# Kernel optimization log

Hardware: AMD Instinct MI355X
Metric: run time of the kernel (lower is better)

The kernel has to match this reference:

```python
import math
import jax, jax.numpy as jnp
import numpy as np

T, B, F = 2048, 8, 768
N_HEAD = 12            # only used for the scale, per original code
N_CHUNK = 3            # chunk(3, -1) -> 3 effective heads
SCALE = math.sqrt(F // N_HEAD)  # sqrt(64) = 8.0


def setup_inputs() -> dict:
    key = jax.random.key(0)
    ks = jax.random.split(key, 9)
    s = 1.0 / math.sqrt(F)
    return {
        "x": jax.random.normal(ks[0], (T, B, F), jnp.float32),
        "Wq": jax.random.normal(ks[1], (F, F), jnp.float32) * s,
        "bq": jax.random.normal(ks[2], (F,), jnp.float32) * s,
        "Wk": jax.random.normal(ks[3], (F, F), jnp.float32) * s,
        "bk": jax.random.normal(ks[4], (F,), jnp.float32) * s,
        "Wv": jax.random.normal(ks[5], (F, F), jnp.float32) * s,
        "bv": jax.random.normal(ks[6], (F,), jnp.float32) * s,
        "Wo": jax.random.normal(ks[7], (F, F), jnp.float32) * s,
        "bo": jax.random.normal(ks[8], (F,), jnp.float32) * s,
    }


def reference(x, Wq, bq, Wk, bk, Wv, bv, Wo, bo):
    # x: (T, B, F). Linear is y = x @ W.T + b (torch convention).
    t, b, f = x.shape
    dh = f // N_CHUNK
    scale = jnp.asarray(SCALE, x.dtype)
    # project then split into 3 chunks along feature dim -> (T, B, 3, dh)
    q = (x @ Wq.T + bq).reshape(t, b, N_CHUNK, dh)
    k = (x @ Wk.T + bk).reshape(t, b, N_CHUNK, dh)
    v = (x @ Wv.T + bv).reshape(t, b, N_CHUNK, dh)
    # scores: (B, H, T, T)
    scores = jnp.einsum('tbhd,sbhd->bhts', q, k) / scale
    attn = jax.nn.softmax(scores, axis=-1)
    # output: (T, B, H, dh) -> (T, B, F)
    o = jnp.einsum('bhts,sbhd->tbhd', attn, v).reshape(t, b, f)
    return o @ Wo.T + bo
```

## Files before the change

kernel.cpp:

```cpp
#include <hip/hip_runtime.h>
#include <cstdint>
#include <cstddef>

#define T_SEQ 2048
#define B_SZ  8
#define F_DIM 768
#define H_CNT 3
#define DH    256

typedef float floatx4 __attribute__((ext_vector_type(4)));
typedef short bf16x8  __attribute__((ext_vector_type(8)));

static __device__ __forceinline__ unsigned short f2bf(float f) {
    union { float f; unsigned int i; } x; x.f = f;
    return (unsigned short)((x.i + 0x8000u) >> 16);
}
static __device__ __forceinline__ unsigned int pkbf(float a, float b) {
    union { float f; unsigned int i; } xa, xb; xa.f = a; xb.f = b;
    return __builtin_amdgcn_perm(xb.i + 0x8000u, xa.i + 0x8000u, 0x07060302u);
}
static __device__ __forceinline__ bf16x8 cvt8(const float* __restrict__ p) {
    const floatx4 a = *(const floatx4*)p;
    const floatx4 b = *(const floatx4*)(p + 4);
    union { unsigned int u[4]; bf16x8 v; } r;
    r.u[0] = pkbf(a[0], a[1]); r.u[1] = pkbf(a[2], a[3]);
    r.u[2] = pkbf(b[0], b[1]); r.u[3] = pkbf(b[2], b[3]);
    return r.v;
}

#define ASYNC16(g, l) __builtin_amdgcn_global_load_lds( \
    (__attribute__((address_space(1))) void*)(void*)(g), \
    (__attribute__((address_space(3))) void*)(l), 16, 0, 0)

template<int AMODE, int CMODE>
__global__ __launch_bounds__(256, 2) void gemm_nt(
    const void* __restrict__ Av,
    const float* __restrict__ W,
    const float* __restrict__ bias,
    void* __restrict__ Cv,
    int M, int N, int K, float scale)
{
    __shared__ __align__(16) unsigned short As[128 * 32];
    __shared__ __align__(16) unsigned short Bs[128 * 32];

    const int tid  = threadIdx.x;
    const int wave = tid >> 6;
    const int lane = tid & 63;
    const int m0 = blockIdx.y * 128;
    const int n0 = blockIdx.x * 128;
    const int wm = (wave >> 1) * 64;
    const int wn = (wave & 1) * 64;
    const int q4 = lane >> 4;
    const int rr = lane & 15;

    const int lrow = lane >> 2;
    const int lk8  = (lane & 3) * 8;
    const int ar0 = wave * 16 + lrow;
    const int ar1 = (wave + 4) * 16 + lrow;

    floatx4 acc[4][4];
#pragma unroll
    for (int i = 0; i < 4; ++i)
#pragma unroll
        for (int j = 0; j < 4; ++j) acc[i][j] = (floatx4)0.0f;

    for (int k0 = 0; k0 < K; k0 += 32) {
        bf16x8 a0, a1;
        if (AMODE == 0) {
            const float* A = (const float*)Av;
            a0 = cvt8(A + (size_t)(m0 + ar0) * K + k0 + lk8);
            a1 = cvt8(A + (size_t)(m0 + ar1) * K + k0 + lk8);
        }
        bf16x8 b0 = cvt8(W + (size_t)(n0 + ar0) * K + k0 + lk8);
        bf16x8 b1 = cvt8(W + (size_t)(n0 + ar1) * K + k0 + lk8);
        __syncthreads();
        if (AMODE == 0) {
            *(bf16x8*)&As[ar0 * 32 + lk8] = a0;
            *(bf16x8*)&As[ar1 * 32 + lk8] = a1;
        } else {
            const unsigned short* A = (const unsigned short*)Av;
            ASYNC16(A + (size_t)(m0 + ar0) * K + k0 + lk8, (unsigned short*)As + wave * 512);
            ASYNC16(A + (size_t)(m0 + ar1) * K + k0 + lk8, (unsigned short*)As + (wave + 4) * 512);
        }
        *(bf16x8*)&Bs[ar0 * 32 + lk8] = b0;
        *(bf16x8*)&Bs[ar1 * 32 + lk8] = b1;
        __syncthreads();

        bf16x8 af[4], bfv[4];
#pragma unroll
        for (int mt = 0; mt < 4; ++mt)
            af[mt] = *(const bf16x8*)&As[(wm + mt * 16 + rr) * 32 + q4 * 8];
#pragma unroll
        for (int nt = 0; nt < 4; ++nt)
            bfv[nt] = *(const bf16x8*)&Bs[(wn + nt * 16 + rr) * 32 + q4 * 8];
#pragma unroll
        for (int mt = 0; mt < 4; ++mt)
#pragma unroll
            for (int nt = 0; nt < 4; ++nt)
                acc[mt][nt] = __builtin_amdgcn_mfma_f32_16x16x32_bf16(af[mt], bfv[nt], acc[mt][nt], 0, 0, 0);
    }

#pragma unroll
    for (int nt = 0; nt < 4; ++nt) {
        const int col = n0 + wn + nt * 16 + rr;
        const float bv = bias[col];
#pragma unroll
        for (int mt = 0; mt < 4; ++mt) {
#pragma unroll
            for (int r = 0; r < 4; ++r) {
                const int row = m0 + wm + mt * 16 + q4 * 4 + r;
                const float v = (acc[mt][nt][r] + bv) * scale;
                if (CMODE == 2) {
                    ((float*)Cv)[(size_t)row * N + col] = v;
                } else {
                    const int t = row >> 3, bb = row & 7;
                    const int h = col >> 8, d = col & 255;
                    const size_t hb = (size_t)(bb * H_CNT + h) * (T_SEQ * DH);
                    size_t idx;
                    if (CMODE == 3) {
                        const int sblk = t >> 4, rrq = t & 15;
                        const int kc = d >> 5, q4v = (d >> 3) & 3, e = d & 7;
                        idx = hb + (size_t)(((sblk * 8 + kc) * 64 + q4v * 16 + rrq) * 8 + e);
                    } else {
                        const int skc = t >> 5, q4v = (t >> 3) & 3, e = t & 7;
                        const int dblk = d >> 4, rrq = d & 15;
                        idx = hb + (size_t)(((skc * 16 + dblk) * 64 + q4v * 16 + rrq) * 8 + e);
                    }
                    ((unsigned short*)Cv)[idx] = f2bf(v);
                }
            }
        }
    }
}

__global__ __launch_bounds__(128, 2) void attn_kernel(
    const unsigned short* __restrict__ Qf,
    const unsigned short* __restrict__ Kf,
    const unsigned short* __restrict__ Vf,
    unsigned short* __restrict__ Ob)
{
    __shared__ __align__(16) unsigned short Ks[8192];
    __shared__ __align__(16) unsigned short Vs[8192];
    __shared__ __align__(16) unsigned short Ps[2][32 * 40];

    const int tid  = threadIdx.x;
    const int wave = tid >> 6;
    const int lane = tid & 63;
    const int q4 = lane >> 4;
    const int rr = lane & 15;
    const int bh = blockIdx.y;
    const int b  = bh / H_CNT;
    const int h  = bh % H_CNT;
    const size_t hb = (size_t)bh * (T_SEQ * DH);

    const int sb0 = blockIdx.x * 4 + wave * 2;
    bf16x8 qf_[2][8];
#pragma unroll
    for (int qnt = 0; qnt < 2; ++qnt)
#pragma unroll
        for (int kc = 0; kc < 8; ++kc)
            qf_[qnt][kc] = *(const bf16x8*)(Qf + hb + ((size_t)((sb0 + qnt) * 8 + kc) * 64 + lane) * 8);

    float m_[2] = { -1e9f, -1e9f }, l_[2] = { 0.0f, 0.0f };
    floatx4 oacc[16][2];
#pragma unroll
    for (int dt = 0; dt < 16; ++dt)
#pragma unroll
        for (int qnt = 0; qnt < 2; ++qnt) oacc[dt][qnt] = (floatx4)0.0f;

    const int sbase = wave * 4096 + lane * 8;

    for (int s0 = 0; s0 < T_SEQ; s0 += 32) {
        const unsigned short* kg = Kf + hb + (size_t)(s0 >> 4) * 4096;
        const unsigned short* vg = Vf + hb + (size_t)(s0 >> 5) * 8192;
#pragma unroll
        for (int rnd = 0; rnd < 8; ++rnd) {
            ASYNC16(kg + sbase + rnd * 512, (unsigned short*)Ks + wave * 4096 + rnd * 512);
            ASYNC16(vg + sbase + rnd * 512, (unsigned short*)Vs + wave * 4096 + rnd * 512);
        }
        __syncthreads();

        floatx4 sacc[2][2];
#pragma unroll
        for (int i = 0; i < 2; ++i)
#pragma unroll
            for (int j = 0; j < 2; ++j) sacc[i][j] = (floatx4)0.0f;
#pragma unroll
        for (int kc = 0; kc < 8; ++kc) {
            bf16x8 k0 = *(const bf16x8*)&Ks[((0 * 8 + kc) * 64 + lane) * 8];
            bf16x8 k1 = *(const bf16x8*)&Ks[((1 * 8 + kc) * 64 + lane) * 8];
            sacc[0][0] = __builtin_amdgcn_mfma_f32_16x16x32_bf16(k0, qf_[0][kc], sacc[0][0], 0, 0, 0);
            sacc[0][1] = __builtin_amdgcn_mfma_f32_16x16x32_bf16(k0, qf_[1][kc], sacc[0][1], 0, 0, 0);
            sacc[1][0] = __builtin_amdgcn_mfma_f32_16x16x32_bf16(k1, qf_[0][kc], sacc[1][0], 0, 0, 0);
            sacc[1][1] = __builtin_amdgcn_mfma_f32_16x16x32_bf16(k1, qf_[1][kc], sacc[1][1], 0, 0, 0);
        }

        float alpha[2];
        int upd = 0;
#pragma unroll
        for (int qnt = 0; qnt < 2; ++qnt) {
            float cm = sacc[0][qnt][0];
#pragma unroll
            for (int smt = 0; smt < 2; ++smt)
#pragma unroll
                for (int r = 0; r < 4; ++r) cm = fmaxf(cm, sacc[smt][qnt][r]);
            cm = fmaxf(cm, __shfl_xor(cm, 16));
            cm = fmaxf(cm, __shfl_xor(cm, 32));
            const float mn = fmaxf(m_[qnt], cm);
            alpha[qnt] = __expf(m_[qnt] - mn);
            float rs = 0.0f;
#pragma unroll
            for (int smt = 0; smt < 2; ++smt)
#pragma unroll
                for (int r = 0; r < 4; ++r) {
                    const float p = __expf(sacc[smt][qnt][r] - mn);
                    sacc[smt][qnt][r] = p; rs += p;
                }
            rs += __shfl_xor(rs, 16);
            rs += __shfl_xor(rs, 32);
            l_[qnt] = alpha[qnt] * l_[qnt] + rs;
            upd |= (mn > m_[qnt]);
            m_[qnt] = mn;
        }

        unsigned short* pw = Ps[wave];
#pragma unroll
        for (int qnt = 0; qnt < 2; ++qnt)
#pragma unroll
            for (int smt = 0; smt < 2; ++smt)
#pragma unroll
                for (int r = 0; r < 4; ++r)
                    pw[(qnt * 16 + rr) * 40 + smt * 16 + q4 * 4 + r] = f2bf(sacc[smt][qnt][r]);
        bf16x8 pf0 = *(const bf16x8*)&pw[(0 * 16 + rr) * 40 + q4 * 8];
        bf16x8 pf1 = *(const bf16x8*)&pw[(1 * 16 + rr) * 40 + q4 * 8];

        if (__any(upd)) {
#pragma unroll
            for (int dt = 0; dt < 16; ++dt)
#pragma unroll
                for (int qnt = 0; qnt < 2; ++qnt)
#pragma unroll
                    for (int r = 0; r < 4; ++r) oacc[dt][qnt][r] *= alpha[qnt];
        }

#pragma unroll
        for (int dt = 0; dt < 16; ++dt) {
            bf16x8 vf = *(const bf16x8*)&Vs[(dt * 64 + lane) * 8];
            oacc[dt][0] = __builtin_amdgcn_mfma_f32_16x16x32_bf16(vf, pf0, oacc[dt][0], 0, 0, 0);
            oacc[dt][1] = __builtin_amdgcn_mfma_f32_16x16x32_bf16(vf, pf1, oacc[dt][1], 0, 0, 0);
        }
        __syncthreads();
    }

#pragma unroll
    for (int qnt = 0; qnt < 2; ++qnt) {
        const float inv_l = 1.0f / fmaxf(l_[qnt], 1e-30f);
        const int t = blockIdx.x * 64 + wave * 32 + qnt * 16 + rr;
        unsigned short* orow = Ob + (size_t)(t * B_SZ + b) * F_DIM + h * DH;
#pragma unroll
        for (int dt = 0; dt < 16; ++dt) {
#pragma unroll
            for (int rp = 0; rp < 2; ++rp) {
                const unsigned int w = pkbf(oacc[dt][qnt][rp * 2] * inv_l,
                                            oacc[dt][qnt][rp * 2 + 1] * inv_l);
                *(unsigned int*)(orow + dt * 16 + q4 * 4 + rp * 2) = w;
            }
        }
    }
}

extern "C" void kernel_launch(void* const* d_in, const int* in_sizes, int n_in,
                              void* d_out, int out_size, void* d_ws, size_t ws_size,
                              hipStream_t stream)
{
    const float* x  = (const float*)d_in[0];
    const float* Wq = (const float*)d_in[1];
    const float* bq = (const float*)d_in[2];
    const float* Wk = (const float*)d_in[3];
    const float* bk = (const float*)d_in[4];
    const float* Wv = (const float*)d_in[5];
    const float* bv = (const float*)d_in[6];
    const float* Wo = (const float*)d_in[7];
    const float* bo = (const float*)d_in[8];
    float* out = (float*)d_out;

    const int M = T_SEQ * B_SZ;
    const int N = F_DIM, K = F_DIM;
    const size_t E = (size_t)M * F_DIM;

    unsigned short* Qf = (unsigned short*)d_ws;
    unsigned short* Kb = Qf + E;
    unsigned short* Vb = Kb + E;
    unsigned short* Ob = Vb + E;

    dim3 g(N / 128, M / 128), blk(256);
    gemm_nt<0, 3><<<g, blk, 0, stream>>>(x, Wq, bq, Qf, M, N, K, 0.125f);
    gemm_nt<0, 3><<<g, blk, 0, stream>>>(x, Wk, bk, Kb, M, N, K, 1.0f);
    gemm_nt<0, 4><<<g, blk, 0, stream>>>(x, Wv, bv, Vb, M, N, K, 1.0f);
    attn_kernel<<<dim3(T_SEQ / 64, B_SZ * H_CNT), dim3(128), 0, stream>>>(Qf, Kb, Vb, Ob);
    gemm_nt<1, 2><<<g, blk, 0, stream>>>(Ob, Wo, bo, out, M, N, K, 1.0f);
}
```

Before: 473.5 us.

## Pre-convert inputs to bf16, batch QKV GEMMs, double-buffer attention K/V loads

Adds a single conversion kernel that turns x and all four weight matrices into bf16 in workspace. The GEMMs can then stream A and B tiles into LDS with async global-to-LDS loads instead of converting fp32 in registers, and the three QKV projections run as one launch over grid z. The attention kernel double-buffers K/V tiles so the next chunk loads while the current one computes, and drops one barrier per iteration. In exchange it adds an extra pass over x, uses more workspace and twice the LDS in attention, which may lower occupancy.

Result: slower. 539.5 us (+13.9%).

```diff
diff --git a/kernel.cpp b/kernel.cpp
--- a/kernel.cpp
+++ b/kernel.cpp
@@ -7,6 +7,7 @@
 #define F_DIM 768
 #define H_CNT 3
 #define DH    256
+#define WSZ   (F_DIM * F_DIM)
 
 typedef float floatx4 __attribute__((ext_vector_type(4)));
 typedef short bf16x8  __attribute__((ext_vector_type(8)));
@@ -19,29 +20,55 @@
     union { float f; unsigned int i; } xa, xb; xa.f = a; xb.f = b;
     return __builtin_amdgcn_perm(xb.i + 0x8000u, xa.i + 0x8000u, 0x07060302u);
 }
-static __device__ __forceinline__ bf16x8 cvt8(const float* __restrict__ p) {
-    const floatx4 a = *(const floatx4*)p;
-    const floatx4 b = *(const floatx4*)(p + 4);
-    union { unsigned int u[4]; bf16x8 v; } r;
-    r.u[0] = pkbf(a[0], a[1]); r.u[1] = pkbf(a[2], a[3]);
-    r.u[2] = pkbf(b[0], b[1]); r.u[3] = pkbf(b[2], b[3]);
-    return r.v;
-}
 
 #define ASYNC16(g, l) __builtin_amdgcn_global_load_lds( \
     (__attribute__((address_space(1))) void*)(void*)(g), \
     (__attribute__((address_space(3))) void*)(l), 16, 0, 0)
 
-template<int AMODE, int CMODE>
-__global__ __launch_bounds__(256, 2) void gemm_nt(
-    const void* __restrict__ Av,
-    const float* __restrict__ W,
-    const float* __restrict__ bias,
+__global__ void cvt_bf16(const float* __restrict__ x,
+                         const float* __restrict__ wq,
+                         const float* __restrict__ wk,
+                         const float* __restrict__ wv,
+                         const float* __restrict__ wo,
+                         unsigned short* __restrict__ dst)
+{
+    const size_t E = (size_t)T_SEQ * B_SZ * F_DIM;
+    const size_t tot8 = (E + 4 * (size_t)WSZ) / 8;
+    for (size_t i = (size_t)blockIdx.x * blockDim.x + threadIdx.x; i < tot8;
+         i += (size_t)gridDim.x * blockDim.x) {
+        const size_t e = i * 8;
+        const float* src; size_t off;
+        if (e < E)                        { src = x;  off = e; }
+        else if (e < E + WSZ)             { src = wq; off = e - E; }
+        else if (e < E + 2 * (size_t)WSZ) { src = wk; off = e - E - WSZ; }
+        else if (e < E + 3 * (size_t)WSZ) { src = wv; off = e - E - 2 * (size_t)WSZ; }
+        else                              { src = wo; off = e - E - 3 * (size_t)WSZ; }
+        const floatx4 a = *(const floatx4*)(src + off);
+        const floatx4 b = *(const floatx4*)(src + off + 4);
+        union { unsigned int u[4]; bf16x8 v; } r;
+        r.u[0] = pkbf(a[0], a[1]); r.u[1] = pkbf(a[2], a[3]);
+        r.u[2] = pkbf(b[0], b[1]); r.u[3] = pkbf(b[2], b[3]);
+        *(bf16x8*)(dst + e) = r.v;
+    }
+}
+
+template<int MODE>
+__global__ __launch_bounds__(256, 2) void gemm_bf16(
+    const unsigned short* __restrict__ A,
+    const unsigned short* __restrict__ Wb,
+    const float* __restrict__ b0,
+    const float* __restrict__ b1,
+    const float* __restrict__ b2,
     void* __restrict__ Cv,
-    int M, int N, int K, float scale)
+    int M, int N, int K)
 {
     __shared__ __align__(16) unsigned short As[128 * 32];
     __shared__ __align__(16) unsigned short Bs[128 * 32];
+
+    const int z    = (MODE == 1) ? blockIdx.z : 0;
+    const unsigned short* W = Wb + (size_t)z * WSZ;
+    const float* bias = (MODE == 1) ? (z == 0 ? b0 : (z == 1 ? b1 : b2)) : b0;
+    const float scale = (MODE == 1 && z == 0) ? 0.125f : 1.0f;
 
     const int tid  = threadIdx.x;
     const int wave = tid >> 6;
@@ -65,25 +92,11 @@
         for (int j = 0; j < 4; ++j) acc[i][j] = (floatx4)0.0f;
 
     for (int k0 = 0; k0 < K; k0 += 32) {
-        bf16x8 a0, a1;
-        if (AMODE == 0) {
-            const float* A = (const float*)Av;
-            a0 = cvt8(A + (size_t)(m0 + ar0) * K + k0 + lk8);
-            a1 = cvt8(A + (size_t)(m0 + ar1) * K + k0 + lk8);
-        }
-        bf16x8 b0 = cvt8(W + (size_t)(n0 + ar0) * K + k0 + lk8);
-        bf16x8 b1 = cvt8(W + (size_t)(n0 + ar1) * K + k0 + lk8);
         __syncthreads();
-        if (AMODE == 0) {
-            *(bf16x8*)&As[ar0 * 32 + lk8] = a0;
-            *(bf16x8*)&As[ar1 * 32 + lk8] = a1;
-        } else {
-            const unsigned short* A = (const unsigned short*)Av;
-            ASYNC16(A + (size_t)(m0 + ar0) * K + k0 + lk8, (unsigned short*)As + wave * 512);
-            ASYNC16(A + (size_t)(m0 + ar1) * K + k0 + lk8, (unsigned short*)As + (wave + 4) * 512);
-        }
-        *(bf16x8*)&Bs[ar0 * 32 + lk8] = b0;
-        *(bf16x8*)&Bs[ar1 * 32 + lk8] = b1;
+        ASYNC16(A + (size_t)(m0 + ar0) * K + k0 + lk8, (unsigned short*)As + wave * 512);
+        ASYNC16(A + (size_t)(m0 + ar1) * K + k0 + lk8, (unsigned short*)As + (wave + 4) * 512);
+        ASYNC16(W + (size_t)(n0 + ar0) * K + k0 + lk8, (unsigned short*)Bs + wave * 512);
+        ASYNC16(W + (size_t)(n0 + ar1) * K + k0 + lk8, (unsigned short*)Bs + (wave + 4) * 512);
         __syncthreads();
 
         bf16x8 af[4], bfv[4];
@@ -110,14 +123,14 @@
             for (int r = 0; r < 4; ++r) {
                 const int row = m0 + wm + mt * 16 + q4 * 4 + r;
                 const float v = (acc[mt][nt][r] + bv) * scale;
-                if (CMODE == 2) {
+                if (MODE == 0) {
                     ((float*)Cv)[(size_t)row * N + col] = v;
                 } else {
                     const int t = row >> 3, bb = row & 7;
                     const int h = col >> 8, d = col & 255;
                     const size_t hb = (size_t)(bb * H_CNT + h) * (T_SEQ * DH);
                     size_t idx;
-                    if (CMODE == 3) {
+                    if (z < 2) {
                         const int sblk = t >> 4, rrq = t & 15;
                         const int kc = d >> 5, q4v = (d >> 3) & 3, e = d & 7;
                         idx = hb + (size_t)(((sblk * 8 + kc) * 64 + q4v * 16 + rrq) * 8 + e);
@@ -126,7 +139,7 @@
                         const int dblk = d >> 4, rrq = d & 15;
                         idx = hb + (size_t)(((skc * 16 + dblk) * 64 + q4v * 16 + rrq) * 8 + e);
                     }
-                    ((unsigned short*)Cv)[idx] = f2bf(v);
+                    ((unsigned short*)Cv + (size_t)z * ((size_t)T_SEQ * B_SZ * F_DIM))[idx] = f2bf(v);
                 }
             }
         }
@@ -139,8 +152,8 @@
     const unsigned short* __restrict__ Vf,
     unsigned short* __restrict__ Ob)
 {
-    __shared__ __align__(16) unsigned short Ks[8192];
-    __shared__ __align__(16) unsigned short Vs[8192];
+    __shared__ __align__(16) unsigned short Ks[2][8192];
+    __shared__ __align__(16) unsigned short Vs[2][8192];
     __shared__ __align__(16) unsigned short Ps[2][32 * 40];
 
     const int tid  = threadIdx.x;
@@ -168,27 +181,38 @@
 #pragma unroll
         for (int qnt = 0; qnt < 2; ++qnt) oacc[dt][qnt] = (floatx4)0.0f;
 
-    const int sbase = wave * 4096 + lane * 8;
-
-    for (int s0 = 0; s0 < T_SEQ; s0 += 32) {
-        const unsigned short* kg = Kf + hb + (size_t)(s0 >> 4) * 4096;
-        const unsigned short* vg = Vf + hb + (size_t)(s0 >> 5) * 8192;
-#pragma unroll
-        for (int rnd = 0; rnd < 8; ++rnd) {
-            ASYNC16(kg + sbase + rnd * 512, (unsigned short*)Ks + wave * 4096 + rnd * 512);
-            ASYNC16(vg + sbase + rnd * 512, (unsigned short*)Vs + wave * 4096 + rnd * 512);
-        }
+    const unsigned short* kg = Kf + hb;
+    const unsigned short* vg = Vf + hb;
+    const int so = wave * 4096 + lane * 8;
+
+#pragma unroll
+    for (int rnd = 0; rnd < 8; ++rnd) {
+        ASYNC16(kg + so + rnd * 512, (unsigned short*)Ks[0] + wave * 4096 + rnd * 512);
+        ASYNC16(vg + so + rnd * 512, (unsigned short*)Vs[0] + wave * 4096 + rnd * 512);
+    }
+
+    for (int i = 0; i < 64; ++i) {
         __syncthreads();
+        const int cur = i & 1;
+        if (i < 63) {
+            const unsigned short* kg2 = kg + (size_t)(i + 1) * 8192;
+            const unsigned short* vg2 = vg + (size_t)(i + 1) * 8192;
+#pragma unroll
+            for (int rnd = 0; rnd < 8; ++rnd) {
+                ASYNC16(kg2 + so + rnd * 512, (unsigned short*)Ks[cur ^ 1] + wave * 4096 + rnd * 512);
+                ASYNC16(vg2 + so + rnd * 512, (unsigned short*)Vs[cur ^ 1] + wave * 4096 + rnd * 512);
+            }
+        }
 
         floatx4 sacc[2][2];
 #pragma unroll
-        for (int i = 0; i < 2; ++i)
-#pragma unroll
-            for (int j = 0; j < 2; ++j) sacc[i][j] = (floatx4)0.0f;
+        for (int a = 0; a < 2; ++a)
+#pragma unroll
+            for (int c = 0; c < 2; ++c) sacc[a][c] = (floatx4)0.0f;
 #pragma unroll
         for (int kc = 0; kc < 8; ++kc) {
-            bf16x8 k0 = *(const bf16x8*)&Ks[((0 * 8 + kc) * 64 + lane) * 8];
-            bf16x8 k1 = *(const bf16x8*)&Ks[((1 * 8 + kc) * 64 + lane) * 8];
+            bf16x8 k0 = *(const bf16x8*)&Ks[cur][((0 * 8 + kc) * 64 + lane) * 8];
+            bf16x8 k1 = *(const bf16x8*)&Ks[cur][((1 * 8 + kc) * 64 + lane) * 8];
             sacc[0][0] = __builtin_amdgcn_mfma_f32_16x16x32_bf16(k0, qf_[0][kc], sacc[0][0], 0, 0, 0);
             sacc[0][1] = __builtin_amdgcn_mfma_f32_16x16x32_bf16(k0, qf_[1][kc], sacc[0][1], 0, 0, 0);
             sacc[1][0] = __builtin_amdgcn_mfma_f32_16x16x32_bf16(k1, qf_[0][kc], sacc[1][0], 0, 0, 0);
@@ -245,11 +269,10 @@
 
 #pragma unroll
         for (int dt = 0; dt < 16; ++dt) {
-            bf16x8 vf = *(const bf16x8*)&Vs[(dt * 64 + lane) * 8];
+            bf16x8 vf = *(const bf16x8*)&Vs[cur][(dt * 64 + lane) * 8];
             oacc[dt][0] = __builtin_amdgcn_mfma_f32_16x16x32_bf16(vf, pf0, oacc[dt][0], 0, 0, 0);
             oacc[dt][1] = __builtin_amdgcn_mfma_f32_16x16x32_bf16(vf, pf1, oacc[dt][1], 0, 0, 0);
         }
-        __syncthreads();
     }
 
 #pragma unroll
@@ -288,15 +311,17 @@
     const int N = F_DIM, K = F_DIM;
     const size_t E = (size_t)M * F_DIM;
 
-    unsigned short* Qf = (unsigned short*)d_ws;
-    unsigned short* Kb = Qf + E;
-    unsigned short* Vb = Kb + E;
-    unsigned short* Ob = Vb + E;
-
-    dim3 g(N / 128, M / 128), blk(256);
-    gemm_nt<0, 3><<<g, blk, 0, stream>>>(x, Wq, bq, Qf, M, N, K, 0.125f);
-    gemm_nt<0, 3><<<g, blk, 0, stream>>>(x, Wk, bk, Kb, M, N, K, 1.0f);
-    gemm_nt<0, 4><<<g, blk, 0, stream>>>(x, Wv, bv, Vb, M, N, K, 1.0f);
+    unsigned short* Qf  = (unsigned short*)d_ws;
+    unsigned short* Kb  = Qf + E;
+    unsigned short* Vb  = Kb + E;
+    unsigned short* Ob  = Vb + E;
+    unsigned short* xb  = Ob + E;
+    unsigned short* W16 = xb + E;
+
+    cvt_bf16<<<dim3(1024), dim3(256), 0, stream>>>(x, Wq, Wk, Wv, Wo, xb);
+    gemm_bf16<1><<<dim3(N / 128, M / 128, 3), dim3(256), 0, stream>>>(
+        xb, W16, bq, bk, bv, Qf, M, N, K);
     attn_kernel<<<dim3(T_SEQ / 64, B_SZ * H_CNT), dim3(128), 0, stream>>>(Qf, Kb, Vb, Ob);
-    gemm_nt<1, 2><<<g, blk, 0, stream>>>(Ob, Wo, bo, out, M, N, K, 1.0f);
-}
+    gemm_bf16<0><<<dim3(N / 128, M / 128), dim3(256), 0, stream>>>(
+        Ob, W16 + (size_t)3 * WSZ, bo, bo, bo, out, M, N, K);
+}
```
